# Optimization experiments

Measured on AMD Instinct MI355X. Metric: run time of the kernel, lower is better.

Reference implementation:

```python
import jax, jax.numpy as jnp
import numpy as np
from jax import lax

# Production-scale dims: batch, seq_len, tag_size (incl. START/STOP tags)
B, S, T = 512, 512, 64


def setup_inputs() -> dict:
    key = jax.random.key(0)
    k1, k2, k3, k4 = jax.random.split(key, 4)
    feats = jax.random.normal(k1, (B, S, T), dtype=jnp.float32)
    # prefix-contiguous mask (module assumes mask[:, 0] == 1 and length-style masks)
    lengths = jax.random.randint(k2, (B,), S // 2, S + 1)
    mask = jnp.arange(S)[None, :] < lengths[:, None]  # (B, S) bool
    tags = jax.random.randint(k3, (B, S), 0, T - 2)  # gold tags exclude START/STOP
    transitions = jax.random.normal(k4, (T, T), dtype=jnp.float32) * 0.1
    return {"feats": feats, "mask": mask, "tags": tags, "transitions": transitions}


def _crf_nll(feats, transitions, mask, tags):
    b, s, t = feats.shape
    START, STOP = t - 2, t - 1  # START_TAG = -2, STOP_TAG = -1

    # ---- forward (log partition), matches _calculate_PZ ----
    # partition init: scores[0][:, START, :] = feats[:,0,:] + transitions[START, :]
    init = feats[:, 0, :] + transitions[START][None, :]  # (b, t)

    feats_t = jnp.swapaxes(feats, 0, 1)  # (s, b, t)
    mask_t = jnp.swapaxes(mask, 0, 1)    # (s, b)

    def step(partition, inp):
        f_t, m_t = inp  # (b, t), (b,)
        # cur_values[b, from, to] = feats_t[b, to] + transitions[from, to] + partition[b, from]
        cur = partition[:, :, None] + transitions[None, :, :] + f_t[:, None, :]
        new_p = jax.nn.logsumexp(cur, axis=1)  # reduce over 'from' -> (b, t)
        partition = jnp.where(m_t[:, None], new_p, partition)
        return partition, None

    partition, _ = lax.scan(step, init, (feats_t[1:], mask_t[1:]))

    # final transition to STOP
    final = jax.nn.logsumexp(partition[:, :, None] + transitions[None, :, :], axis=1)
    forward_score = final[:, STOP].sum()

    # ---- gold score, matches _score_sentence ----
    prev = jnp.concatenate(
        [jnp.full((b, 1), START, dtype=tags.dtype), tags[:, :-1]], axis=1
    )  # (b, s): previous tag, START at position 0
    emit = jnp.take_along_axis(feats, tags[:, :, None], axis=2)[:, :, 0]  # (b, s)
    tg_energy = emit + transitions[prev, tags]  # (b, s)
    gold = jnp.where(mask, tg_energy, jnp.zeros((), feats.dtype)).sum()
    lengths = mask.sum(axis=1).astype(jnp.int32)  # (b,)
    end_ids = jnp.take_along_axis(tags, (lengths - 1)[:, None].astype(tags.dtype), axis=1)[:, 0]
    gold = gold + transitions[end_ids, STOP].sum()

    # average_batch = False
    return forward_score - gold


def reference(feats, mask, tags, transitions):
    return _crf_nll(feats, transitions, mask, tags)
```

## Files before the change

### kernel.cpp

```cpp
#include <hip/hip_runtime.h>

#define BB 512
#define SS 512
#define TT 64
#define START_TAG 62
#define STOP_TAG 63

#define LOG2E 1.4426950408889634f
#define LN2   0.6931471805599453f

typedef _Float16 h2 __attribute__((ext_vector_type(2)));
typedef _Float16 h8 __attribute__((ext_vector_type(8)));

__device__ __forceinline__ float bcast0(float x) {
    return __int_as_float(__builtin_amdgcn_readfirstlane(__float_as_int(x)));
}

__device__ __forceinline__ float matvec_dot(const _Float16* Ebuf,
                                            const h2 (&Mh)[32]) {
    float a0 = 0.f, a1 = 0.f, a2 = 0.f, a3 = 0.f;
    float a4 = 0.f, a5 = 0.f, a6 = 0.f, a7 = 0.f;
    h8 v[8];
    #pragma unroll
    for (int j = 0; j < 8; ++j) v[j] = *(const h8*)(Ebuf + 8 * j);
    #pragma unroll
    for (int j = 0; j < 8; ++j) {
        const h2 p0 = __builtin_shufflevector(v[j], v[j], 0, 1);
        const h2 p1 = __builtin_shufflevector(v[j], v[j], 2, 3);
        const h2 p2 = __builtin_shufflevector(v[j], v[j], 4, 5);
        const h2 p3 = __builtin_shufflevector(v[j], v[j], 6, 7);
        a0 = __builtin_amdgcn_fdot2(p0, Mh[4 * j + 0], a0, false);
        a1 = __builtin_amdgcn_fdot2(p1, Mh[4 * j + 1], a1, false);
        a2 = __builtin_amdgcn_fdot2(p2, Mh[4 * j + 2], a2, false);
        a3 = __builtin_amdgcn_fdot2(p3, Mh[4 * j + 3], a3, false);
        const float t = a0; a0 = a4; a4 = t;
        const float u = a1; a1 = a5; a5 = u;
        const float w = a2; a2 = a6; a6 = w;
        const float x = a3; a3 = a7; a7 = x;
    }
    return ((a0 + a1) + (a2 + a3)) + ((a4 + a5) + (a6 + a7));
}

#define STEP(FRJ) { \
    const float fe = __builtin_amdgcn_exp2f((FRJ) * LOG2E); \
    const float D  = matvec_dot(Ebuf, Mh); \
    const int eb = (__builtin_amdgcn_readfirstlane(__float_as_int(D)) \
                    >> 23) & 0xff; \
    ksum += eb - 127; \
    const float scale = __int_as_float((254 - eb) << 23); \
    Ebuf[lane] = (_Float16)(fe * (D * scale)); \
}

__global__ void __launch_bounds__(128)
__attribute__((amdgpu_waves_per_eu(1, 1))) crf_main(
    const float* __restrict__ feats, const int* __restrict__ mask,
    const int* __restrict__ tags, const float* __restrict__ trans,
    float* __restrict__ out)
{
    const int b    = blockIdx.x;
    const int tid  = threadIdx.x;
    const int lane = tid & 63;

    const float* frow = feats + (size_t)b * SS * TT;
    const int*   mrow = mask + b * SS;

    __shared__ __align__(16) _Float16 Ebuf[TT];

    if (tid < 64) {
        int cnt = 0;
        #pragma unroll
        for (int s = lane; s < SS; s += 64) cnt += (mrow[s] != 0);
        #pragma unroll
        for (int off = 32; off; off >>= 1) cnt += __shfl_xor(cnt, off);
        const int len = cnt;

        h2 Mh[32];
        #pragma unroll
        for (int p = 0; p < 32; ++p) {
            const float m0 =
                __builtin_amdgcn_exp2f(trans[(2 * p) * TT + lane] * LOG2E);
            const float m1 =
                __builtin_amdgcn_exp2f(trans[(2 * p + 1) * TT + lane] * LOG2E);
            Mh[p][0] = (_Float16)m0;
            Mh[p][1] = (_Float16)m1;
        }

        const float P0   = frow[lane] + trans[START_TAG * TT + lane];
        const float offs = bcast0(P0);
        Ebuf[lane] = (_Float16)__builtin_amdgcn_exp2f((P0 - offs) * LOG2E);
        int ksum = 0;

        float fr[8];
        #pragma unroll
        for (int j = 0; j < 8; ++j) {
            int r = 1 + j; if (r > SS - 1) r = SS - 1;
            fr[j] = frow[(size_t)r * TT + lane];
        }

        int s = 1;
        for (; s + 3 < len; s += 4) {
            float n0, n1, n2, n3;
            {
                int r0 = s + 8, r1 = s + 9, r2 = s + 10, r3 = s + 11;
                if (r0 > SS - 1) r0 = SS - 1;
                if (r1 > SS - 1) r1 = SS - 1;
                if (r2 > SS - 1) r2 = SS - 1;
                if (r3 > SS - 1) r3 = SS - 1;
                n0 = frow[(size_t)r0 * TT + lane];
                n1 = frow[(size_t)r1 * TT + lane];
                n2 = frow[(size_t)r2 * TT + lane];
                n3 = frow[(size_t)r3 * TT + lane];
            }

            STEP(fr[0]) STEP(fr[1]) STEP(fr[2]) STEP(fr[3])

            #pragma unroll
            for (int j = 0; j < 4; ++j) fr[j] = fr[j + 4];
            fr[4] = n0; fr[5] = n1; fr[6] = n2; fr[7] = n3;
        }

        const int rem = len - s;
        if (rem > 0) { STEP(fr[0]) }
        if (rem > 1) { STEP(fr[1]) }
        if (rem > 2) { STEP(fr[2]) }

        const float Ev = (float)Ebuf[lane];
        const float Ms =
            __builtin_amdgcn_exp2f(trans[lane * TT + STOP_TAG] * LOG2E);
        float e = Ev * Ms;
        #pragma unroll
        for (int off = 32; off; off >>= 1) e += __shfl_xor(e, off);

        if (lane == 0)
            atomicAdd(out, offs + (float)ksum * LN2
                           + LN2 * __builtin_amdgcn_logf(e));
    } else {
        const int* trow = tags + b * SS;
        int   cnt = 0;
        float acc = 0.f;
        for (int s = lane; s < SS; s += 64) {
            if (mrow[s] != 0) {
                ++cnt;
                const int tag  = trow[s];
                const int prev = (s == 0) ? START_TAG : trow[s - 1];
                acc += frow[(size_t)s * TT + tag] + trans[prev * TT + tag];
            }
        }
        #pragma unroll
        for (int off = 32; off; off >>= 1) {
            acc += __shfl_xor(acc, off);
            cnt += __shfl_xor(cnt, off);
        }
        if (lane == 0) {
            const int end_id = trow[cnt - 1];
            atomicAdd(out, -(acc + trans[end_id * TT + STOP_TAG]));
        }
    }
}

__global__ void zero_out(float* out) { out[0] = 0.f; }

extern "C" void kernel_launch(void* const* d_in, const int* in_sizes, int n_in,
                              void* d_out, int out_size, void* d_ws, size_t ws_size,
                              hipStream_t stream) {
    const float* feats = (const float*)d_in[0];
    const int*   mask  = (const int*)d_in[1];
    const int*   tags  = (const int*)d_in[2];
    const float* trans = (const float*)d_in[3];
    float* out = (float*)d_out;

    zero_out<<<1, 1, 0, stream>>>(out);
    crf_main<<<BB, 128, 0, stream>>>(feats, mask, tags, trans, out);
}
```

Baseline: 175.1 us.

## Compute CRF forward recurrence matvec with MFMA instead of fdot2 via LDS

Replaces the per-lane fdot2 matvec, which re-read the partition vector from LDS every step, with 16x16x32 f16 MFMA instructions. The exp-transition matrix is held in registers as A fragments and the partition vector lives in the B operand. Output fragments are rescaled, packed to half and multiplied by precomputed exp(feats) staged in a small ring buffer in LDS. This keeps the recurrence in registers and removes the LDS write/read round trip on the serial critical path, at the cost of wasting most MFMA columns on a matrix-vector product. It also replaces the zeroing kernel with hipMemsetAsync.

```diff
diff --git a/kernel.cpp b/kernel.cpp
--- a/kernel.cpp
+++ b/kernel.cpp
@@ -11,44 +11,10 @@
 
 typedef _Float16 h2 __attribute__((ext_vector_type(2)));
 typedef _Float16 h8 __attribute__((ext_vector_type(8)));
-
-__device__ __forceinline__ float bcast0(float x) {
-    return __int_as_float(__builtin_amdgcn_readfirstlane(__float_as_int(x)));
-}
-
-__device__ __forceinline__ float matvec_dot(const _Float16* Ebuf,
-                                            const h2 (&Mh)[32]) {
-    float a0 = 0.f, a1 = 0.f, a2 = 0.f, a3 = 0.f;
-    float a4 = 0.f, a5 = 0.f, a6 = 0.f, a7 = 0.f;
-    h8 v[8];
-    #pragma unroll
-    for (int j = 0; j < 8; ++j) v[j] = *(const h8*)(Ebuf + 8 * j);
-    #pragma unroll
-    for (int j = 0; j < 8; ++j) {
-        const h2 p0 = __builtin_shufflevector(v[j], v[j], 0, 1);
-        const h2 p1 = __builtin_shufflevector(v[j], v[j], 2, 3);
-        const h2 p2 = __builtin_shufflevector(v[j], v[j], 4, 5);
-        const h2 p3 = __builtin_shufflevector(v[j], v[j], 6, 7);
-        a0 = __builtin_amdgcn_fdot2(p0, Mh[4 * j + 0], a0, false);
-        a1 = __builtin_amdgcn_fdot2(p1, Mh[4 * j + 1], a1, false);
-        a2 = __builtin_amdgcn_fdot2(p2, Mh[4 * j + 2], a2, false);
-        a3 = __builtin_amdgcn_fdot2(p3, Mh[4 * j + 3], a3, false);
-        const float t = a0; a0 = a4; a4 = t;
-        const float u = a1; a1 = a5; a5 = u;
-        const float w = a2; a2 = a6; a6 = w;
-        const float x = a3; a3 = a7; a7 = x;
-    }
-    return ((a0 + a1) + (a2 + a3)) + ((a4 + a5) + (a6 + a7));
-}
-
-#define STEP(FRJ) { \
-    const float fe = __builtin_amdgcn_exp2f((FRJ) * LOG2E); \
-    const float D  = matvec_dot(Ebuf, Mh); \
-    const int eb = (__builtin_amdgcn_readfirstlane(__float_as_int(D)) \
-                    >> 23) & 0xff; \
-    ksum += eb - 127; \
-    const float scale = __int_as_float((254 - eb) << 23); \
-    Ebuf[lane] = (_Float16)(fe * (D * scale)); \
+typedef float    f4 __attribute__((ext_vector_type(4)));
+
+__device__ __forceinline__ h2 pkrtz(float a, float b) {
+    return __builtin_bit_cast(h2, __builtin_amdgcn_cvt_pkrtz(a, b));
 }
 
 __global__ void __launch_bounds__(128)
@@ -64,9 +30,12 @@
     const float* frow = feats + (size_t)b * SS * TT;
     const int*   mrow = mask + b * SS;
 
-    __shared__ __align__(16) _Float16 Ebuf[TT];
+    __shared__ __align__(16) _Float16 febuf[8][TT];
 
     if (tid < 64) {
+        const int g  = lane >> 4;
+        const int cg = lane & 15;
+
         int cnt = 0;
         #pragma unroll
         for (int s = lane; s < SS; s += 64) cnt += (mrow[s] != 0);
@@ -74,21 +43,31 @@
         for (int off = 32; off; off >>= 1) cnt += __shfl_xor(cnt, off);
         const int len = cnt;
 
-        h2 Mh[32];
-        #pragma unroll
-        for (int p = 0; p < 32; ++p) {
-            const float m0 =
-                __builtin_amdgcn_exp2f(trans[(2 * p) * TT + lane] * LOG2E);
-            const float m1 =
-                __builtin_amdgcn_exp2f(trans[(2 * p + 1) * TT + lane] * LOG2E);
-            Mh[p][0] = (_Float16)m0;
-            Mh[p][1] = (_Float16)m1;
-        }
-
-        const float P0   = frow[lane] + trans[START_TAG * TT + lane];
-        const float offs = bcast0(P0);
-        Ebuf[lane] = (_Float16)__builtin_amdgcn_exp2f((P0 - offs) * LOG2E);
+        const int to_base   = 16 * (cg >> 2) + (cg & 3);
+        const int from_base = 16 * g;
+        h8 A[4][2];
+        #pragma unroll
+        for (int tt = 0; tt < 4; ++tt)
+            #pragma unroll
+            for (int kc = 0; kc < 2; ++kc)
+                #pragma unroll
+                for (int j = 0; j < 8; ++j)
+                    A[tt][kc][j] = (_Float16)__builtin_amdgcn_exp2f(
+                        trans[(from_base + 8 * kc + j) * TT
+                              + (to_base + 4 * tt)] * LOG2E);
+
+        const float offs = frow[0] + trans[START_TAG * TT + 0];
+        h8 B0, B1;
+        #pragma unroll
+        for (int sl = 0; sl < 8; ++sl) {
+            const int t0 = 16 * g + sl, t1 = t0 + 8;
+            B0[sl] = (_Float16)__builtin_amdgcn_exp2f(
+                (frow[t0] + trans[START_TAG * TT + t0] - offs) * LOG2E);
+            B1[sl] = (_Float16)__builtin_amdgcn_exp2f(
+                (frow[t1] + trans[START_TAG * TT + t1] - offs) * LOG2E);
+        }
         int ksum = 0;
+        const f4 Z = {0.f, 0.f, 0.f, 0.f};
 
         float fr[8];
         #pragma unroll
@@ -96,6 +75,52 @@
             int r = 1 + j; if (r > SS - 1) r = SS - 1;
             fr[j] = frow[(size_t)r * TT + lane];
         }
+        #pragma unroll
+        for (int j = 0; j < 4; ++j)
+            febuf[(1 + j) & 7][lane] =
+                (_Float16)__builtin_amdgcn_exp2f(fr[j] * LOG2E);
+
+        auto step = [&](int row) {
+            const _Float16* fb = &febuf[row & 7][16 * g];
+            const h8 fe0 = *(const h8*)(fb);
+            const h8 fe1 = *(const h8*)(fb + 8);
+            f4 d0 = __builtin_amdgcn_mfma_f32_16x16x32_f16(A[0][0], B0, Z, 0, 0, 0);
+            f4 d1 = __builtin_amdgcn_mfma_f32_16x16x32_f16(A[1][0], B0, Z, 0, 0, 0);
+            f4 d2 = __builtin_amdgcn_mfma_f32_16x16x32_f16(A[2][0], B0, Z, 0, 0, 0);
+            f4 d3 = __builtin_amdgcn_mfma_f32_16x16x32_f16(A[3][0], B0, Z, 0, 0, 0);
+            d0 = __builtin_amdgcn_mfma_f32_16x16x32_f16(A[0][1], B1, d0, 0, 0, 0);
+            d1 = __builtin_amdgcn_mfma_f32_16x16x32_f16(A[1][1], B1, d1, 0, 0, 0);
+            d2 = __builtin_amdgcn_mfma_f32_16x16x32_f16(A[2][1], B1, d2, 0, 0, 0);
+            d3 = __builtin_amdgcn_mfma_f32_16x16x32_f16(A[3][1], B1, d3, 0, 0, 0);
+            const int eb = (__builtin_amdgcn_readfirstlane(
+                                __float_as_int(d0[0])) >> 23) & 0xff;
+            ksum += eb - 127;
+            const float sc = __int_as_float((254 - eb) << 23);
+            const h2 p0 = pkrtz(d0[0] * sc, d0[1] * sc);
+            const h2 p1 = pkrtz(d0[2] * sc, d0[3] * sc);
+            const h2 p2 = pkrtz(d1[0] * sc, d1[1] * sc);
+            const h2 p3 = pkrtz(d1[2] * sc, d1[3] * sc);
+            const h2 p4 = pkrtz(d2[0] * sc, d2[1] * sc);
+            const h2 p5 = pkrtz(d2[2] * sc, d2[3] * sc);
+            const h2 p6 = pkrtz(d3[0] * sc, d3[1] * sc);
+            const h2 p7 = pkrtz(d3[2] * sc, d3[3] * sc);
+            const h2 q0 = p0 * __builtin_shufflevector(fe0, fe0, 0, 1);
+            const h2 q1 = p1 * __builtin_shufflevector(fe0, fe0, 2, 3);
+            const h2 q2 = p2 * __builtin_shufflevector(fe0, fe0, 4, 5);
+            const h2 q3 = p3 * __builtin_shufflevector(fe0, fe0, 6, 7);
+            const h2 q4 = p4 * __builtin_shufflevector(fe1, fe1, 0, 1);
+            const h2 q5 = p5 * __builtin_shufflevector(fe1, fe1, 2, 3);
+            const h2 q6 = p6 * __builtin_shufflevector(fe1, fe1, 4, 5);
+            const h2 q7 = p7 * __builtin_shufflevector(fe1, fe1, 6, 7);
+            B0 = __builtin_shufflevector(
+                     __builtin_shufflevector(q0, q1, 0, 1, 2, 3),
+                     __builtin_shufflevector(q2, q3, 0, 1, 2, 3),
+                     0, 1, 2, 3, 4, 5, 6, 7);
+            B1 = __builtin_shufflevector(
+                     __builtin_shufflevector(q4, q5, 0, 1, 2, 3),
+                     __builtin_shufflevector(q6, q7, 0, 1, 2, 3),
+                     0, 1, 2, 3, 4, 5, 6, 7);
+        };
 
         int s = 1;
         for (; s + 3 < len; s += 4) {
@@ -111,8 +136,16 @@
                 n2 = frow[(size_t)r2 * TT + lane];
                 n3 = frow[(size_t)r3 * TT + lane];
             }
-
-            STEP(fr[0]) STEP(fr[1]) STEP(fr[2]) STEP(fr[3])
+            febuf[(s + 4) & 7][lane] =
+                (_Float16)__builtin_amdgcn_exp2f(fr[4] * LOG2E);
+            febuf[(s + 5) & 7][lane] =
+                (_Float16)__builtin_amdgcn_exp2f(fr[5] * LOG2E);
+            febuf[(s + 6) & 7][lane] =
+                (_Float16)__builtin_amdgcn_exp2f(fr[6] * LOG2E);
+            febuf[(s + 7) & 7][lane] =
+                (_Float16)__builtin_amdgcn_exp2f(fr[7] * LOG2E);
+
+            step(s); step(s + 1); step(s + 2); step(s + 3);
 
             #pragma unroll
             for (int j = 0; j < 4; ++j) fr[j] = fr[j + 4];
@@ -120,16 +153,21 @@
         }
 
         const int rem = len - s;
-        if (rem > 0) { STEP(fr[0]) }
-        if (rem > 1) { STEP(fr[1]) }
-        if (rem > 2) { STEP(fr[2]) }
-
-        const float Ev = (float)Ebuf[lane];
-        const float Ms =
-            __builtin_amdgcn_exp2f(trans[lane * TT + STOP_TAG] * LOG2E);
-        float e = Ev * Ms;
-        #pragma unroll
-        for (int off = 32; off; off >>= 1) e += __shfl_xor(e, off);
+        if (rem > 0) step(s);
+        if (rem > 1) step(s + 1);
+        if (rem > 2) step(s + 2);
+
+        float e = 0.f;
+        #pragma unroll
+        for (int sl = 0; sl < 8; ++sl) {
+            const int t0 = 16 * g + sl, t1 = t0 + 8;
+            e += (float)B0[sl] * __builtin_amdgcn_exp2f(
+                     trans[t0 * TT + STOP_TAG] * LOG2E);
+            e += (float)B1[sl] * __builtin_amdgcn_exp2f(
+                     trans[t1 * TT + STOP_TAG] * LOG2E);
+        }
+        e += __shfl_xor(e, 16);
+        e += __shfl_xor(e, 32);
 
         if (lane == 0)
             atomicAdd(out, offs + (float)ksum * LN2
@@ -158,8 +196,6 @@
     }
 }
 
-__global__ void zero_out(float* out) { out[0] = 0.f; }
-
 extern "C" void kernel_launch(void* const* d_in, const int* in_sizes, int n_in,
                               void* d_out, int out_size, void* d_ws, size_t ws_size,
                               hipStream_t stream) {
@@ -169,6 +205,6 @@
     const float* trans = (const float*)d_in[3];
     float* out = (float*)d_out;
 
-    zero_out<<<1, 1, 0, stream>>>(out);
+    (void)hipMemsetAsync(out, 0, sizeof(float), stream);
     crf_main<<<BB, 128, 0, stream>>>(feats, mask, tags, trans, out);
 }
```

Result: slower. 186.4 us (+6.5%).
